# Kernel optimization log

Hardware: AMD Instinct MI355X
Metric: run time of the kernel (lower is better)

The kernel has to match this reference:

```python
import math
import jax, jax.numpy as jnp
import numpy as np

LAMDA = 0.5
ALPHA = 0.1
N_NODES = 100000
N_EDGES = 1600000
NFEAT = 512
NHID = 128
NCLASS = 40
NLAYER = 4


def setup_inputs() -> dict:
    key = jax.random.key(0)
    ks = jax.random.split(key, 9)
    x = jax.random.normal(ks[0], (N_NODES, NFEAT), dtype=jnp.float32)
    rows = jnp.sort(jax.random.randint(ks[1], (N_EDGES,), 0, N_NODES, dtype=jnp.int32))
    cols = jax.random.randint(ks[2], (N_EDGES,), 0, N_NODES, dtype=jnp.int32)
    # positive edge weights (stand-in for symmetric-normalized adjacency values)
    vals = jax.random.uniform(ks[3], (N_EDGES,), dtype=jnp.float32) * 0.1
    stdv_hid = 1.0 / math.sqrt(NHID)
    fc1_w = jax.random.normal(ks[4], (NFEAT, NHID), dtype=jnp.float32) * 0.02
    fc1_b = jnp.zeros((NHID,), dtype=jnp.float32)
    conv_w = jax.random.uniform(ks[5], (NLAYER, NHID, NHID), dtype=jnp.float32,
                                minval=-stdv_hid, maxval=stdv_hid)
    fc2_w = jax.random.normal(ks[6], (NHID, NCLASS), dtype=jnp.float32) * 0.02
    fc2_b = jnp.zeros((NCLASS,), dtype=jnp.float32)
    return {"x": x, "rows": rows, "cols": cols, "vals": vals,
            "fc1_w": fc1_w, "fc1_b": fc1_b, "conv_w": conv_w,
            "fc2_w": fc2_w, "fc2_b": fc2_b}


def reference(x, rows, cols, vals, fc1_w, fc1_b, conv_w, fc2_w, fc2_b):
    n = x.shape[0]
    # input projection + relu (dropout is identity in eval mode)
    h = jax.nn.relu(x @ fc1_w + fc1_b)  # [N, nhid]
    h0 = h
    for i in range(conv_w.shape[0]):
        theta = math.log(LAMDA / (i + 1) + 1.0)
        # sparse spmm: hi = A @ h  via gather + segment-sum scatter
        hi = jax.ops.segment_sum(vals[:, None] * h[cols], rows, num_segments=n)
        support = (1.0 - ALPHA) * hi + ALPHA * h0  # initial-residual mix
        h = jax.nn.relu(theta * (support @ conv_w[i]) + (1.0 - theta) * support)
    logits = h @ fc2_w + fc2_b  # [N, nclass]
    return (jax.nn.log_softmax(logits, axis=1), h, jnp.concatenate([h, logits], axis=1))
```

## Files before the change

kernel.cpp:

```cpp
#include <hip/hip_runtime.h>
#include <math.h>

#define N_NODES 100000
#define NFEAT 512
#define NHID 128
#define NCLASS 40

typedef unsigned int uint;
typedef unsigned short ushort;
typedef short bf16x8 __attribute__((ext_vector_type(8)));
typedef float f32x4 __attribute__((ext_vector_type(4)));

__device__ inline ushort bf16s(float a) {
    uint u = __float_as_uint(a);
    return (ushort)((u + 0x7fffu + ((u >> 16) & 1u)) >> 16);
}
__device__ inline uint bf16pack(float a, float b) {
    return (uint)bf16s(a) | ((uint)bf16s(b) << 16);
}
__device__ inline float bf16tof(ushort u) { return __uint_as_float(((uint)u) << 16); }
__device__ inline float bflo(uint u) { return __uint_as_float(u << 16); }
__device__ inline float bfhi(uint u) { return __uint_as_float(u & 0xffff0000u); }

__global__ void prep_weights(const float* __restrict__ fc1_w, const float* __restrict__ conv_w,
                             ushort* __restrict__ wT1, ushort* __restrict__ wTc) {
    int idx = blockIdx.x * 256 + threadIdx.x;
    {   int n = idx >> 9, k = idx & 511;
        wT1[idx] = bf16s(fc1_w[k * NHID + n]); }
    {   int L = idx >> 14, rem = idx & 16383;
        int n = rem >> 7, k = rem & 127;
        wTc[idx] = bf16s(conv_w[L * 16384 + k * NHID + n]); }
}

__global__ void rowptr_kernel(const int* __restrict__ rows, int* __restrict__ rowptr, int nE) {
    int i = blockIdx.x * blockDim.x + threadIdx.x;
    if (i > N_NODES) return;
    int lo = 0, hi = nE;
    while (lo < hi) { int mid = (lo + hi) >> 1; if (rows[mid] < i) lo = mid + 1; else hi = mid; }
    rowptr[i] = lo;
}

__global__ void __launch_bounds__(256) fc1_mfma(const float* __restrict__ x,
                                                const uint* __restrict__ wT1,
                                                const float* __restrict__ bias,
                                                ushort* __restrict__ h0b) {
    __shared__ ushort As[32][72];
    __shared__ ushort Bs[128][72];
    const int tid = threadIdx.x;
    const int lane = tid & 63;
    const int wave = tid >> 6;
    const int wr = wave >> 1, wc = wave & 1;
    const int r0 = blockIdx.x * 32;

    f32x4 acc[4] = {};

    for (int ks = 0; ks < NFEAT; ks += 64) {
        {
            int row = tid >> 3, kq = tid & 7;
            const float* xp = x + (size_t)(r0 + row) * NFEAT + ks + kq * 8;
            float4 v0 = *reinterpret_cast<const float4*>(xp);
            float4 v1 = *reinterpret_cast<const float4*>(xp + 4);
            uint4 pk;
            pk.x = bf16pack(v0.x, v0.y); pk.y = bf16pack(v0.z, v0.w);
            pk.z = bf16pack(v1.x, v1.y); pk.w = bf16pack(v1.z, v1.w);
            *reinterpret_cast<uint4*>(&As[row][kq * 8]) = pk;
        }
        #pragma unroll
        for (int p = 0; p < 4; ++p) {
            int idx = tid + p * 256;
            int n = idx >> 3, q = idx & 7;
            uint4 w4 = *reinterpret_cast<const uint4*>(wT1 + n * 256 + (ks >> 1) + q * 4);
            *reinterpret_cast<uint4*>(&Bs[n][q * 8]) = w4;
        }
        __syncthreads();
        #pragma unroll
        for (int ks2 = 0; ks2 < 64; ks2 += 32) {
            bf16x8 a = *reinterpret_cast<const bf16x8*>(&As[wr * 16 + (lane & 15)][ks2 + (lane >> 4) * 8]);
            #pragma unroll
            for (int j = 0; j < 4; ++j) {
                bf16x8 b = *reinterpret_cast<const bf16x8*>(&Bs[wc * 64 + j * 16 + (lane & 15)][ks2 + (lane >> 4) * 8]);
                acc[j] = __builtin_amdgcn_mfma_f32_16x16x32_bf16(a, b, acc[j], 0, 0, 0);
            }
        }
        __syncthreads();
    }

    const int cb = wc * 64 + (lane & 15);
    const int rb = r0 + wr * 16 + ((lane >> 4) << 2);
    #pragma unroll
    for (int j = 0; j < 4; ++j) {
        int col = cb + j * 16;
        float bj = bias[col];
        #pragma unroll
        for (int i = 0; i < 4; ++i) {
            float v = fmaxf(acc[j][i] + bj, 0.f);
            h0b[(size_t)(rb + i) * NHID + col] = bf16s(v);
        }
    }
}

__global__ void __launch_bounds__(256) layer_mfma(const uint* __restrict__ sb,
                                                  const uint* __restrict__ wTc,
                                                  float theta,
                                                  ushort* __restrict__ hb,
                                                  float* __restrict__ fout) {
    __shared__ ushort As[32][136];
    __shared__ ushort Bs[128][136];
    const int tid = threadIdx.x;
    const int lane = tid & 63;
    const int wave = tid >> 6;
    const int wr = wave >> 1, wc = wave & 1;
    const int r0 = blockIdx.x * 32;

    #pragma unroll
    for (int p = 0; p < 2; ++p) {
        int idx = tid + p * 256;
        int row = idx >> 4, kq = idx & 15;
        uint4 v = *reinterpret_cast<const uint4*>(sb + (size_t)(r0 + row) * 64 + kq * 4);
        *reinterpret_cast<uint4*>(&As[row][kq * 8]) = v;
    }
    #pragma unroll
    for (int p = 0; p < 8; ++p) {
        int idx = tid + p * 256;
        int n = idx >> 4, kq = idx & 15;
        uint4 v = *reinterpret_cast<const uint4*>(wTc + n * 64 + kq * 4);
        *reinterpret_cast<uint4*>(&Bs[n][kq * 8]) = v;
    }
    __syncthreads();

    f32x4 acc[4] = {};
    #pragma unroll
    for (int ks = 0; ks < NHID; ks += 32) {
        bf16x8 a = *reinterpret_cast<const bf16x8*>(&As[wr * 16 + (lane & 15)][ks + (lane >> 4) * 8]);
        #pragma unroll
        for (int j = 0; j < 4; ++j) {
            bf16x8 b = *reinterpret_cast<const bf16x8*>(&Bs[wc * 64 + j * 16 + (lane & 15)][ks + (lane >> 4) * 8]);
            acc[j] = __builtin_amdgcn_mfma_f32_16x16x32_bf16(a, b, acc[j], 0, 0, 0);
        }
    }

    const float om = 1.f - theta;
    const int cb = wc * 64 + (lane & 15);
    const int rloc = wr * 16 + ((lane >> 4) << 2);
    #pragma unroll
    for (int j = 0; j < 4; ++j) {
        int col = cb + j * 16;
        #pragma unroll
        for (int i = 0; i < 4; ++i) {
            float s = bf16tof(As[rloc + i][col]);
            float v = fmaxf(fmaf(theta, acc[j][i], om * s), 0.f);
            if (fout) fout[(size_t)(r0 + rloc + i) * NHID + col] = v;
            else      hb[(size_t)(r0 + rloc + i) * NHID + col] = bf16s(v);
        }
    }
}

__global__ void spmm_kernel(const uint2* __restrict__ hb2, const uint2* __restrict__ h0b2,
                            const int* __restrict__ rowptr, const int* __restrict__ cols,
                            const float* __restrict__ vals, uint2* __restrict__ sb2) {
    const int node = blockIdx.x * 4 + (threadIdx.x >> 6);
    const int lane = threadIdx.x & 63;
    const int half = lane >> 5;
    const int l    = lane & 31;

    const int e0 = rowptr[node], e1 = rowptr[node + 1];

    float a0 = 0.f, a1 = 0.f, a2 = 0.f, a3 = 0.f;
    for (int base = e0; base < e1; base += 64) {
        int m = e1 - base; if (m > 64) m = 64;
        int c = 0; float v = 0.f;
        if (lane < m) { c = cols[base + lane]; v = vals[base + lane]; }
        const int nt = (m + 1) >> 1;
        #pragma unroll 8
        for (int t = 0; t < nt; ++t) {
            int j = 2 * t + half;
            int jc = (j < m) ? j : 0;
            int   cj = __shfl(c, jc);
            float vj = __shfl(v, jc);
            if (j >= m) vj = 0.f;
            uint2 hv = hb2[(size_t)cj * 32 + l];
            a0 = fmaf(vj, bflo(hv.x), a0);
            a1 = fmaf(vj, bfhi(hv.x), a1);
            a2 = fmaf(vj, bflo(hv.y), a2);
            a3 = fmaf(vj, bfhi(hv.y), a3);
        }
    }
    a0 += __shfl_xor(a0, 32);
    a1 += __shfl_xor(a1, 32);
    a2 += __shfl_xor(a2, 32);
    a3 += __shfl_xor(a3, 32);

    if (half == 0) {
        uint2 h0v = h0b2[(size_t)node * 32 + l];
        float o0 = 0.9f * a0 + 0.1f * bflo(h0v.x);
        float o1 = 0.9f * a1 + 0.1f * bfhi(h0v.x);
        float o2 = 0.9f * a2 + 0.1f * bflo(h0v.y);
        float o3 = 0.9f * a3 + 0.1f * bfhi(h0v.y);
        uint2 o; o.x = bf16pack(o0, o1); o.y = bf16pack(o2, o3);
        sb2[(size_t)node * 32 + l] = o;
    }
}

__global__ void final_kernel(const float* __restrict__ h, const float* __restrict__ w,
                             const float* __restrict__ b, float* __restrict__ out0,
                             float* __restrict__ out2) {
    __shared__ float hs[4][128];
    const int s = threadIdx.x >> 6;
    const int lane = threadIdx.x & 63;
    const int node = blockIdx.x * 4 + s;

    float h_lo = h[node * NHID + lane];
    float h_hi = h[node * NHID + 64 + lane];
    hs[s][lane] = h_lo;
    hs[s][64 + lane] = h_hi;
    __syncthreads();

    float logit = 0.f;
    if (lane < NCLASS) {
        logit = b[lane];
        #pragma unroll 8
        for (int k = 0; k < NHID; ++k)
            logit = fmaf(hs[s][k], w[k * NCLASS + lane], logit);
    }

    float mv = (lane < NCLASS) ? logit : -1e30f;
    #pragma unroll
    for (int m = 32; m; m >>= 1) mv = fmaxf(mv, __shfl_xor(mv, m));
    float ev = (lane < NCLASS) ? __expf(logit - mv) : 0.f;
    float sum = ev;
    #pragma unroll
    for (int m = 32; m; m >>= 1) sum += __shfl_xor(sum, m);
    float lse = mv + __logf(sum);

    if (lane < NCLASS) {
        out0[node * NCLASS + lane] = logit - lse;
        out2[node * 168 + 128 + lane] = logit;
    }
    out2[node * 168 + lane] = h_lo;
    out2[node * 168 + 64 + lane] = h_hi;
}

extern "C" void kernel_launch(void* const* d_in, const int* in_sizes, int n_in,
                              void* d_out, int out_size, void* d_ws, size_t ws_size,
                              hipStream_t stream) {
    const float* x      = (const float*)d_in[0];
    const int*   rows   = (const int*)  d_in[1];
    const int*   cols   = (const int*)  d_in[2];
    const float* vals   = (const float*)d_in[3];
    const float* fc1_w  = (const float*)d_in[4];
    const float* fc1_b  = (const float*)d_in[5];
    const float* conv_w = (const float*)d_in[6];
    const float* fc2_w  = (const float*)d_in[7];
    const float* fc2_b  = (const float*)d_in[8];
    float* out = (float*)d_out;

    const int nE = in_sizes[1];
    const size_t NH = (size_t)N_NODES * NHID;

    char* p = (char*)d_ws;
    int*    rowptr = (int*)p;          p += 400128;
    ushort* h0b    = (ushort*)p;       p += NH * 2;
    ushort* hb     = (ushort*)p;       p += NH * 2;
    ushort* sb     = (ushort*)p;       p += NH * 2;
    ushort* wT1    = (ushort*)p;       p += 65536 * 2;
    ushort* wTc    = (ushort*)p;       p += 65536 * 2;

    float* out0 = out;
    float* out1 = out + (size_t)N_NODES * NCLASS;
    float* out2 = out1 + NH;

    prep_weights<<<256, 256, 0, stream>>>(fc1_w, conv_w, wT1, wTc);
    rowptr_kernel<<<(N_NODES + 1 + 255) / 256, 256, 0, stream>>>(rows, rowptr, nE);
    fc1_mfma<<<N_NODES / 32, 256, 0, stream>>>(x, (const uint*)wT1, fc1_b, h0b);

    for (int i = 0; i < 4; ++i) {
        float theta = logf(0.5f / (float)(i + 1) + 1.0f);
        spmm_kernel<<<N_NODES / 4, 256, 0, stream>>>(
            (const uint2*)(i == 0 ? h0b : hb), (const uint2*)h0b, rowptr, cols, vals, (uint2*)sb);
        layer_mfma<<<N_NODES / 32, 256, 0, stream>>>(
            (const uint*)sb, (const uint*)(wTc + (size_t)i * 16384), theta,
            (i < 3) ? hb : nullptr, (i == 3) ? out1 : nullptr);
    }

    final_kernel<<<N_NODES / 4, 256, 0, stream>>>(out1, fc2_w, fc2_b, out0, out2);
}
```

Before: 543.7 us.

## Widen SpMM gathers to 16-byte loads and double layer GEMM row tile

The SpMM kernel now splits each wave into four 16-lane groups, each loading a whole 128-wide bf16 row with uint4 gathers, so four edges are processed per step and the result is reduced with two shuffle stages. The layer GEMM block now covers 64 rows instead of 32, so each staged weight tile is reused across twice as many rows. It uses a bounds guard and padded workspace buffers for the partial last block. The intent is fewer, wider memory transactions in the gather and less per-block weight staging, at the cost of more registers and LDS per block.

```diff
diff --git a/kernel.cpp b/kernel.cpp
--- a/kernel.cpp
+++ b/kernel.cpp
@@ -55,8 +55,7 @@
     f32x4 acc[4] = {};
 
     for (int ks = 0; ks < NFEAT; ks += 64) {
-        {
-            int row = tid >> 3, kq = tid & 7;
+        {   int row = tid >> 3, kq = tid & 7;
             const float* xp = x + (size_t)(r0 + row) * NFEAT + ks + kq * 8;
             float4 v0 = *reinterpret_cast<const float4*>(xp);
             float4 v1 = *reinterpret_cast<const float4*>(xp + 4);
@@ -104,16 +103,16 @@
                                                   float theta,
                                                   ushort* __restrict__ hb,
                                                   float* __restrict__ fout) {
-    __shared__ ushort As[32][136];
+    __shared__ ushort As[64][136];
     __shared__ ushort Bs[128][136];
     const int tid = threadIdx.x;
     const int lane = tid & 63;
     const int wave = tid >> 6;
     const int wr = wave >> 1, wc = wave & 1;
-    const int r0 = blockIdx.x * 32;
-
-    #pragma unroll
-    for (int p = 0; p < 2; ++p) {
+    const int r0 = blockIdx.x * 64;
+
+    #pragma unroll
+    for (int p = 0; p < 4; ++p) {
         int idx = tid + p * 256;
         int row = idx >> 4, kq = idx & 15;
         uint4 v = *reinterpret_cast<const uint4*>(sb + (size_t)(r0 + row) * 64 + kq * 4);
@@ -128,76 +127,94 @@
     }
     __syncthreads();
 
-    f32x4 acc[4] = {};
+    f32x4 acc[2][4] = {};
     #pragma unroll
     for (int ks = 0; ks < NHID; ks += 32) {
-        bf16x8 a = *reinterpret_cast<const bf16x8*>(&As[wr * 16 + (lane & 15)][ks + (lane >> 4) * 8]);
-        #pragma unroll
-        for (int j = 0; j < 4; ++j) {
-            bf16x8 b = *reinterpret_cast<const bf16x8*>(&Bs[wc * 64 + j * 16 + (lane & 15)][ks + (lane >> 4) * 8]);
-            acc[j] = __builtin_amdgcn_mfma_f32_16x16x32_bf16(a, b, acc[j], 0, 0, 0);
+        #pragma unroll
+        for (int mr = 0; mr < 2; ++mr) {
+            bf16x8 a = *reinterpret_cast<const bf16x8*>(&As[wr * 32 + mr * 16 + (lane & 15)][ks + (lane >> 4) * 8]);
+            #pragma unroll
+            for (int j = 0; j < 4; ++j) {
+                bf16x8 b = *reinterpret_cast<const bf16x8*>(&Bs[wc * 64 + j * 16 + (lane & 15)][ks + (lane >> 4) * 8]);
+                acc[mr][j] = __builtin_amdgcn_mfma_f32_16x16x32_bf16(a, b, acc[mr][j], 0, 0, 0);
+            }
         }
     }
 
     const float om = 1.f - theta;
     const int cb = wc * 64 + (lane & 15);
-    const int rloc = wr * 16 + ((lane >> 4) << 2);
-    #pragma unroll
-    for (int j = 0; j < 4; ++j) {
-        int col = cb + j * 16;
-        #pragma unroll
-        for (int i = 0; i < 4; ++i) {
-            float s = bf16tof(As[rloc + i][col]);
-            float v = fmaxf(fmaf(theta, acc[j][i], om * s), 0.f);
-            if (fout) fout[(size_t)(r0 + rloc + i) * NHID + col] = v;
-            else      hb[(size_t)(r0 + rloc + i) * NHID + col] = bf16s(v);
-        }
-    }
-}
-
-__global__ void spmm_kernel(const uint2* __restrict__ hb2, const uint2* __restrict__ h0b2,
+    #pragma unroll
+    for (int mr = 0; mr < 2; ++mr) {
+        const int rloc = wr * 32 + mr * 16 + ((lane >> 4) << 2);
+        #pragma unroll
+        for (int j = 0; j < 4; ++j) {
+            int col = cb + j * 16;
+            #pragma unroll
+            for (int i = 0; i < 4; ++i) {
+                int gr = r0 + rloc + i;
+                if (gr < N_NODES) {
+                    float s = bf16tof(As[rloc + i][col]);
+                    float v = fmaxf(fmaf(theta, acc[mr][j][i], om * s), 0.f);
+                    if (fout) fout[(size_t)gr * NHID + col] = v;
+                    else      hb[(size_t)gr * NHID + col] = bf16s(v);
+                }
+            }
+        }
+    }
+}
+
+__global__ void spmm_kernel(const uint4* __restrict__ hb4, const uint4* __restrict__ h0b4,
                             const int* __restrict__ rowptr, const int* __restrict__ cols,
-                            const float* __restrict__ vals, uint2* __restrict__ sb2) {
+                            const float* __restrict__ vals, uint4* __restrict__ sb4) {
     const int node = blockIdx.x * 4 + (threadIdx.x >> 6);
     const int lane = threadIdx.x & 63;
-    const int half = lane >> 5;
-    const int l    = lane & 31;
+    const int q = lane >> 4;
+    const int l = lane & 15;
 
     const int e0 = rowptr[node], e1 = rowptr[node + 1];
 
     float a0 = 0.f, a1 = 0.f, a2 = 0.f, a3 = 0.f;
+    float a4 = 0.f, a5 = 0.f, a6 = 0.f, a7 = 0.f;
     for (int base = e0; base < e1; base += 64) {
         int m = e1 - base; if (m > 64) m = 64;
         int c = 0; float v = 0.f;
         if (lane < m) { c = cols[base + lane]; v = vals[base + lane]; }
-        const int nt = (m + 1) >> 1;
+        const int nt = (m + 3) >> 2;
         #pragma unroll 8
         for (int t = 0; t < nt; ++t) {
-            int j = 2 * t + half;
+            int j = 4 * t + q;
             int jc = (j < m) ? j : 0;
             int   cj = __shfl(c, jc);
             float vj = __shfl(v, jc);
             if (j >= m) vj = 0.f;
-            uint2 hv = hb2[(size_t)cj * 32 + l];
+            uint4 hv = hb4[(size_t)cj * 16 + l];
             a0 = fmaf(vj, bflo(hv.x), a0);
             a1 = fmaf(vj, bfhi(hv.x), a1);
             a2 = fmaf(vj, bflo(hv.y), a2);
             a3 = fmaf(vj, bfhi(hv.y), a3);
-        }
-    }
-    a0 += __shfl_xor(a0, 32);
-    a1 += __shfl_xor(a1, 32);
-    a2 += __shfl_xor(a2, 32);
-    a3 += __shfl_xor(a3, 32);
-
-    if (half == 0) {
-        uint2 h0v = h0b2[(size_t)node * 32 + l];
-        float o0 = 0.9f * a0 + 0.1f * bflo(h0v.x);
-        float o1 = 0.9f * a1 + 0.1f * bfhi(h0v.x);
-        float o2 = 0.9f * a2 + 0.1f * bflo(h0v.y);
-        float o3 = 0.9f * a3 + 0.1f * bfhi(h0v.y);
-        uint2 o; o.x = bf16pack(o0, o1); o.y = bf16pack(o2, o3);
-        sb2[(size_t)node * 32 + l] = o;
+            a4 = fmaf(vj, bflo(hv.z), a4);
+            a5 = fmaf(vj, bfhi(hv.z), a5);
+            a6 = fmaf(vj, bflo(hv.w), a6);
+            a7 = fmaf(vj, bfhi(hv.w), a7);
+        }
+    }
+    a0 += __shfl_xor(a0, 16); a1 += __shfl_xor(a1, 16);
+    a2 += __shfl_xor(a2, 16); a3 += __shfl_xor(a3, 16);
+    a4 += __shfl_xor(a4, 16); a5 += __shfl_xor(a5, 16);
+    a6 += __shfl_xor(a6, 16); a7 += __shfl_xor(a7, 16);
+    a0 += __shfl_xor(a0, 32); a1 += __shfl_xor(a1, 32);
+    a2 += __shfl_xor(a2, 32); a3 += __shfl_xor(a3, 32);
+    a4 += __shfl_xor(a4, 32); a5 += __shfl_xor(a5, 32);
+    a6 += __shfl_xor(a6, 32); a7 += __shfl_xor(a7, 32);
+
+    if (q == 0) {
+        uint4 h0v = h0b4[(size_t)node * 16 + l];
+        uint4 o;
+        o.x = bf16pack(0.9f * a0 + 0.1f * bflo(h0v.x), 0.9f * a1 + 0.1f * bfhi(h0v.x));
+        o.y = bf16pack(0.9f * a2 + 0.1f * bflo(h0v.y), 0.9f * a3 + 0.1f * bfhi(h0v.y));
+        o.z = bf16pack(0.9f * a4 + 0.1f * bflo(h0v.z), 0.9f * a5 + 0.1f * bfhi(h0v.z));
+        o.w = bf16pack(0.9f * a6 + 0.1f * bflo(h0v.w), 0.9f * a7 + 0.1f * bfhi(h0v.w));
+        sb4[(size_t)node * 16 + l] = o;
     }
 }
 
@@ -256,12 +273,13 @@
 
     const int nE = in_sizes[1];
     const size_t NH = (size_t)N_NODES * NHID;
+    const size_t PAD = 64 * NHID;
 
     char* p = (char*)d_ws;
     int*    rowptr = (int*)p;          p += 400128;
     ushort* h0b    = (ushort*)p;       p += NH * 2;
-    ushort* hb     = (ushort*)p;       p += NH * 2;
-    ushort* sb     = (ushort*)p;       p += NH * 2;
+    ushort* hb     = (ushort*)p;       p += (NH + PAD) * 2;
+    ushort* sb     = (ushort*)p;       p += (NH + PAD) * 2;
     ushort* wT1    = (ushort*)p;       p += 65536 * 2;
     ushort* wTc    = (ushort*)p;       p += 65536 * 2;
 
@@ -276,8 +294,8 @@
     for (int i = 0; i < 4; ++i) {
         float theta = logf(0.5f / (float)(i + 1) + 1.0f);
         spmm_kernel<<<N_NODES / 4, 256, 0, stream>>>(
-            (const uint2*)(i == 0 ? h0b : hb), (const uint2*)h0b, rowptr, cols, vals, (uint2*)sb);
-        layer_mfma<<<N_NODES / 32, 256, 0, stream>>>(
+            (const uint4*)(i == 0 ? h0b : hb), (const uint4*)h0b, rowptr, cols, vals, (uint4*)sb);
+        layer_mfma<<<(N_NODES + 63) / 64, 256, 0, stream>>>(
             (const uint*)sb, (const uint*)(wTc + (size_t)i * 16384), theta,
             (i < 3) ? hb : nullptr, (i == 3) ? out1 : nullptr);
     }
```

Measured after the change: 501.2 us. 7.8% less time.
